# Kernel optimization log

Hardware: AMD Instinct MI355X
Metric: run time of the kernel (lower is better)

## Reference

```python
import jax, jax.numpy as jnp
import numpy as np

H0, H1, NHID, BATCH = 256, 256, 512, 2048

def setup_inputs() -> dict:
    key = jax.random.key(0)
    k1, k2, k3, k4, k5 = jax.random.split(key, 5)
    initrange = 0.1
    inputs = jax.random.normal(k1, (BATCH, NHID), dtype=jnp.float32)
    labels = jax.random.randint(k2, (BATCH,), 0, H1, dtype=jnp.int32)
    parent_labels = jax.random.randint(k3, (BATCH,), 0, H0, dtype=jnp.int32)
    layer_top_W = jax.random.uniform(k4, (NHID, H0), jnp.float32, -initrange, initrange)
    layer_top_b = jnp.zeros((H0,), jnp.float32)
    layer_bottom_W = jax.random.uniform(k5, (H0, NHID, H1), jnp.float32, -initrange, initrange)
    layer_bottom_b = jnp.zeros((H0, H1), jnp.float32)
    return {"inputs": inputs, "labels": labels, "parent_labels": parent_labels,
            "layer_top_W": layer_top_W, "layer_top_b": layer_top_b,
            "layer_bottom_W": layer_bottom_W, "layer_bottom_b": layer_bottom_b}

def reference(inputs, labels, parent_labels, layer_top_W, layer_top_b,
              layer_bottom_W, layer_bottom_b):
    batch = inputs.shape[0]
    # top-level softmax over coarse classes: [B, H0]
    top_probs = jax.nn.softmax(inputs @ layer_top_W + layer_top_b, axis=1)
    # per-sample gather of expert weight slice [B, NHID, H1] then bmm
    Wb = layer_bottom_W[parent_labels]            # [B, NHID, H1]
    bb = layer_bottom_b[parent_labels]            # [B, H1]
    bottom_logits = jnp.einsum('bd,bdk->bk', inputs, Wb) + bb
    bottom_probs = jax.nn.softmax(bottom_logits, axis=1)
    ar = jnp.arange(batch)
    target_probs = top_probs[ar, parent_labels] * bottom_probs[ar, labels]
    return target_probs
```

## Files before the change

kernel.cpp:

```cpp
#include <hip/hip_runtime.h>

constexpr int BATCH = 2048;
constexpr int NHID  = 512;
constexpr int H0    = 256;
constexpr int H1    = 256;
constexpr int S     = 8;
constexpr int J     = 3;

__global__ __launch_bounds__(256) void hs_wavelocal(
    const float* __restrict__ x,
    const int*   __restrict__ labels,
    const int*   __restrict__ parents,
    const float* __restrict__ topW,
    const float* __restrict__ topb,
    const float* __restrict__ botW,
    const float* __restrict__ botb,
    float*       __restrict__ out)
{
    const int p = blockIdx.x & 255;
    const int j = blockIdx.x >> 8;
    const int t = threadIdx.x;
    const int g = t >> 6;
    const int l = t & 63;
    const int mypass = g >> 1;
    const int sb     = (g & 1) * 4;

    __shared__ int   list[BATCH];
    __shared__ int   wcnt[4];
    __shared__ __align__(16) float xs[S][NHID];
    __shared__ float psm[2][S];

    int running = 0;
    for (int c = 0; c < BATCH; c += 256) {
        const bool match = (parents[c + t] == p);
        const unsigned long long mask = __ballot(match);
        if (l == 0) wcnt[g] = __popcll(mask);
        __syncthreads();
        int off = running;
        for (int w = 0; w < g; ++w) off += wcnt[w];
        if (match)
            list[off + __popcll(mask & ((1ull << l) - 1ull))] = c + t;
        running += wcnt[0] + wcnt[1] + wcnt[2] + wcnt[3];
        __syncthreads();
    }
    const int n = running;
    if (n <= j * S) return;

    const float* Wbase = mypass ? botW + (size_t)p * NHID * H1 : topW;
    const float4 b4    = mypass ? *(const float4*)(botb + (size_t)p * H1 + 4 * l)
                                : *(const float4*)(topb + 4 * l);

    for (int base = j * S; base < n; base += J * S) {
        const int rem = min(S, n - base);

        for (int s = 0; s < S; ++s) {
            const int idx = list[base + min(s, rem - 1)];
            ((float2*)xs[s])[t] = ((const float2*)(x + (size_t)idx * NHID))[t];
        }

        int tgts[4];
        #pragma unroll
        for (int si = 0; si < 4; ++si) {
            const int slot = base + min(sb + si, rem - 1);
            tgts[si] = mypass ? labels[list[slot]] : p;
        }
        __syncthreads();

        float4 acc[4];
        #pragma unroll
        for (int si = 0; si < 4; ++si) acc[si] = make_float4(0.f, 0.f, 0.f, 0.f);

        const float* Wp = Wbase + 4 * l;
        float4 ring[8];
        #pragma unroll
        for (int i = 0; i < 8; ++i)
            ring[i] = *(const float4*)(Wp + (size_t)i * H0);

        for (int d = 0; d < NHID; d += 8) {
            #pragma unroll
            for (int h = 0; h < 2; ++h) {
                const int dd = d + 4 * h;
                float4 w0 = ring[4 * h + 0], w1 = ring[4 * h + 1];
                float4 w2 = ring[4 * h + 2], w3 = ring[4 * h + 3];
                if (dd + 8 < NHID) {
                    #pragma unroll
                    for (int i = 0; i < 4; ++i)
                        ring[4 * h + i] =
                            *(const float4*)(Wp + (size_t)(dd + 8 + i) * H0);
                }
                #pragma unroll
                for (int si = 0; si < 4; ++si) {
                    const float4 xv = *(const float4*)&xs[sb + si][dd];
                    float4 a = acc[si];
                    a.x = fmaf(xv.x, w0.x, a.x); a.y = fmaf(xv.x, w0.y, a.y);
                    a.z = fmaf(xv.x, w0.z, a.z); a.w = fmaf(xv.x, w0.w, a.w);
                    a.x = fmaf(xv.y, w1.x, a.x); a.y = fmaf(xv.y, w1.y, a.y);
                    a.z = fmaf(xv.y, w1.z, a.z); a.w = fmaf(xv.y, w1.w, a.w);
                    a.x = fmaf(xv.z, w2.x, a.x); a.y = fmaf(xv.z, w2.y, a.y);
                    a.z = fmaf(xv.z, w2.z, a.z); a.w = fmaf(xv.z, w2.w, a.w);
                    a.x = fmaf(xv.w, w3.x, a.x); a.y = fmaf(xv.w, w3.y, a.y);
                    a.z = fmaf(xv.w, w3.z, a.z); a.w = fmaf(xv.w, w3.w, a.w);
                    acc[si] = a;
                }
            }
        }

        #pragma unroll
        for (int si = 0; si < 4; ++si) {
            float4 v = acc[si];
            v.x += b4.x; v.y += b4.y; v.z += b4.z; v.w += b4.w;

            float m = fmaxf(fmaxf(v.x, v.y), fmaxf(v.z, v.w));
            #pragma unroll
            for (int off = 32; off > 0; off >>= 1)
                m = fmaxf(m, __shfl_xor(m, off, 64));

            const float ex = expf(v.x - m), ey = expf(v.y - m);
            const float ez = expf(v.z - m), ew = expf(v.w - m);
            float sum = (ex + ey) + (ez + ew);
            #pragma unroll
            for (int off = 32; off > 0; off >>= 1)
                sum += __shfl_xor(sum, off, 64);

            const int tgt = tgts[si];
            const int k   = tgt & 3;
            const float ev = (k == 0) ? ex : (k == 1) ? ey : (k == 2) ? ez : ew;
            if (l == (tgt >> 2))
                psm[mypass][sb + si] = ev / sum;
        }
        __syncthreads();

        if (t < rem) {
            const int idx = list[base + t];
            out[idx] = psm[0][t] * psm[1][t];
        }
        __syncthreads();
    }
}

extern "C" void kernel_launch(void* const* d_in, const int* in_sizes, int n_in,
                              void* d_out, int out_size, void* d_ws, size_t ws_size,
                              hipStream_t stream) {
    const float* x       = (const float*)d_in[0];
    const int*   labels  = (const int*)  d_in[1];
    const int*   parents = (const int*)  d_in[2];
    const float* topW    = (const float*)d_in[3];
    const float* topb    = (const float*)d_in[4];
    const float* botW    = (const float*)d_in[5];
    const float* botb    = (const float*)d_in[6];
    float*       out     = (float*)d_out;

    hs_wavelocal<<<H0 * J, 256, 0, stream>>>(x, labels, parents,
                                             topW, topb, botW, botb, out);
}
```

Before: 239.4 us.

## Halve block to two waves, each computing all eight samples per weight load

Each block now runs one wave per pass (top or bottom) instead of two, and each wave accumulates all 8 samples, so every weight row fetched from memory is reused across twice as many samples. Weight traffic per block drops by half, and x staging switches to float4 loads. Blocks are also reindexed so the J blocks of one parent sit next to each other. The cost is more accumulator registers per thread and fewer waves per block, which may lower occupancy and latency hiding.

```diff
diff --git a/kernel.cpp b/kernel.cpp
--- a/kernel.cpp
+++ b/kernel.cpp
@@ -7,7 +7,7 @@
 constexpr int S     = 8;
 constexpr int J     = 3;
 
-__global__ __launch_bounds__(256) void hs_wavelocal(
+__global__ __launch_bounds__(128) void hs_8s(
     const float* __restrict__ x,
     const int*   __restrict__ labels,
     const int*   __restrict__ parents,
@@ -17,58 +17,55 @@
     const float* __restrict__ botb,
     float*       __restrict__ out)
 {
-    const int p = blockIdx.x & 255;
-    const int j = blockIdx.x >> 8;
+    const int p = blockIdx.x / J;
+    const int j = blockIdx.x % J;
     const int t = threadIdx.x;
     const int g = t >> 6;
     const int l = t & 63;
-    const int mypass = g >> 1;
-    const int sb     = (g & 1) * 4;
 
     __shared__ int   list[BATCH];
-    __shared__ int   wcnt[4];
+    __shared__ int   wcnt[2];
     __shared__ __align__(16) float xs[S][NHID];
     __shared__ float psm[2][S];
 
     int running = 0;
-    for (int c = 0; c < BATCH; c += 256) {
+    for (int c = 0; c < BATCH; c += 128) {
         const bool match = (parents[c + t] == p);
         const unsigned long long mask = __ballot(match);
         if (l == 0) wcnt[g] = __popcll(mask);
         __syncthreads();
-        int off = running;
-        for (int w = 0; w < g; ++w) off += wcnt[w];
+        const int off = running + (g ? wcnt[0] : 0);
         if (match)
             list[off + __popcll(mask & ((1ull << l) - 1ull))] = c + t;
-        running += wcnt[0] + wcnt[1] + wcnt[2] + wcnt[3];
+        running += wcnt[0] + wcnt[1];
         __syncthreads();
     }
     const int n = running;
     if (n <= j * S) return;
 
-    const float* Wbase = mypass ? botW + (size_t)p * NHID * H1 : topW;
-    const float4 b4    = mypass ? *(const float4*)(botb + (size_t)p * H1 + 4 * l)
-                                : *(const float4*)(topb + 4 * l);
+    const float* Wbase = g ? botW + (size_t)p * NHID * H1 : topW;
+    const float4 b4    = g ? *(const float4*)(botb + (size_t)p * H1 + 4 * l)
+                           : *(const float4*)(topb + 4 * l);
 
     for (int base = j * S; base < n; base += J * S) {
         const int rem = min(S, n - base);
 
         for (int s = 0; s < S; ++s) {
             const int idx = list[base + min(s, rem - 1)];
-            ((float2*)xs[s])[t] = ((const float2*)(x + (size_t)idx * NHID))[t];
+            ((float4*)xs[s])[t] = ((const float4*)(x + (size_t)idx * NHID))[t];
         }
 
-        int tgts[4];
+        int tgts[S];
         #pragma unroll
-        for (int si = 0; si < 4; ++si) {
-            const int slot = base + min(sb + si, rem - 1);
-            tgts[si] = mypass ? labels[list[slot]] : p;
+        for (int s = 0; s < S; ++s) {
+            const int slot = base + min(s, rem - 1);
+            tgts[s] = g ? labels[list[slot]] : p;
         }
         __syncthreads();
 
-        float4 acc[4];
+        float4 acc[S];
         #pragma unroll
-        for (int si = 0; si < 4; ++si) acc[si] = make_float4(0.f, 0.f, 0.f, 0.f);
+        for (int s = 0; s < S; ++s) acc[s] = make_float4(0.f, 0.f, 0.f, 0.f);
 
         const float* Wp = Wbase + 4 * l;
         float4 ring[8];
@@ -80,8 +77,8 @@
             #pragma unroll
             for (int h = 0; h < 2; ++h) {
                 const int dd = d + 4 * h;
-                float4 w0 = ring[4 * h + 0], w1 = ring[4 * h + 1];
-                float4 w2 = ring[4 * h + 2], w3 = ring[4 * h + 3];
+                const float4 w0 = ring[4 * h + 0], w1 = ring[4 * h + 1];
+                const float4 w2 = ring[4 * h + 2], w3 = ring[4 * h + 3];
                 if (dd + 8 < NHID) {
                     #pragma unroll
                     for (int i = 0; i < 4; ++i)
@@ -89,9 +86,9 @@
                             *(const float4*)(Wp + (size_t)(dd + 8 + i) * H0);
                 }
                 #pragma unroll
-                for (int si = 0; si < 4; ++si) {
-                    const float4 xv = *(const float4*)&xs[sb + si][dd];
-                    float4 a = acc[si];
+                for (int s = 0; s < S; ++s) {
+                    const float4 xv = *(const float4*)&xs[s][dd];
+                    float4 a = acc[s];
                     a.x = fmaf(xv.x, w0.x, a.x); a.y = fmaf(xv.x, w0.y, a.y);
                     a.z = fmaf(xv.x, w0.z, a.z); a.w = fmaf(xv.x, w0.w, a.w);
                     a.x = fmaf(xv.y, w1.x, a.x); a.y = fmaf(xv.y, w1.y, a.y);
@@ -100,14 +97,14 @@
                     a.z = fmaf(xv.z, w2.z, a.z); a.w = fmaf(xv.z, w2.w, a.w);
                     a.x = fmaf(xv.w, w3.x, a.x); a.y = fmaf(xv.w, w3.y, a.y);
                     a.z = fmaf(xv.w, w3.z, a.z); a.w = fmaf(xv.w, w3.w, a.w);
-                    acc[si] = a;
+                    acc[s] = a;
                 }
             }
         }
 
         #pragma unroll
-        for (int si = 0; si < 4; ++si) {
-            float4 v = acc[si];
+        for (int s = 0; s < S; ++s) {
+            float4 v = acc[s];
             v.x += b4.x; v.y += b4.y; v.z += b4.z; v.w += b4.w;
 
             float m = fmaxf(fmaxf(v.x, v.y), fmaxf(v.z, v.w));
@@ -122,11 +119,11 @@
             for (int off = 32; off > 0; off >>= 1)
                 sum += __shfl_xor(sum, off, 64);
 
-            const int tgt = tgts[si];
+            const int tgt = tgts[s];
             const int k   = tgt & 3;
             const float ev = (k == 0) ? ex : (k == 1) ? ey : (k == 2) ? ez : ew;
             if (l == (tgt >> 2))
-                psm[mypass][sb + si] = ev / sum;
+                psm[g][s] = ev / sum;
         }
         __syncthreads();
 
@@ -150,6 +147,6 @@
     const float* botb    = (const float*)d_in[6];
     float*       out     = (float*)d_out;
 
-    hs_wavelocal<<<H0 * J, 256, 0, stream>>>(x, labels, parents,
-                                             topW, topb, botW, botb, out);
+    hs_8s<<<H0 * J, 128, 0, stream>>>(x, labels, parents,
+                                      topW, topb, botW, botb, out);
 }
```

New measurement: 227.9 us. 1.05x faster.
